# Kernel tuning notes

Measured on AMD Instinct MI355X. Metric: run time of the kernel, lower is better.

The kernel has to match this reference:

```python
import jax, jax.numpy as jnp
import numpy as np

EPS = 1e-7
LN_EPS = 1e-5

N_NODES = 50000
N_EDGES = 1600000
D = 128
L = 3


def layer_norm(h, scale, bias):
    mu = jnp.mean(h, axis=-1, keepdims=True)
    var = jnp.var(h, axis=-1, keepdims=True)
    return (h - mu) * jax.lax.rsqrt(var + LN_EPS) * scale + bias


def gen_conv(h, src, dst, edge_attr, W1, b1, W2, b2, beta, n_nodes):
    # message: ReLU(x_j + edge_attr) + eps   -> [E, D]
    msg = jax.nn.relu(h[src] + edge_attr) + EPS
    # softmax aggregation over incoming edges of each dst node, per feature
    s = beta * msg
    m = jax.ops.segment_max(s, dst, num_segments=n_nodes)  # [N, D]
    e = jnp.exp(s - m[dst])
    den = jax.ops.segment_sum(e, dst, num_segments=n_nodes)  # [N, D]
    alpha = e / den[dst]
    aggr = jax.ops.segment_sum(alpha * msg, dst, num_segments=n_nodes)  # [N, D]
    # MLP(x + aggr): D -> 2D -> D
    out = h + aggr
    out = jax.nn.relu(out @ W1 + b1)
    return out @ W2 + b2


def setup_inputs() -> dict:
    key = jax.random.key(0)
    ks = jax.random.split(key, 8)
    x = jax.random.normal(ks[0], (N_NODES, D), dtype=jnp.float32)
    edge_index = jax.random.randint(ks[1], (2, N_EDGES), 0, N_NODES, dtype=jnp.int64)
    edge_attr = jax.random.normal(ks[2], (N_EDGES, D), dtype=jnp.float32)
    return {
        "x": x,
        "edge_index": edge_index,
        "edge_attr": edge_attr,
        "ln_scale": jnp.ones((L, D), jnp.float32),
        "ln_bias": jnp.zeros((L, D), jnp.float32),
        "W1": jax.random.normal(ks[3], (L, D, 2 * D), jnp.float32) * 0.05,
        "b1": jnp.zeros((L, 2 * D), jnp.float32),
        "W2": jax.random.normal(ks[4], (L, 2 * D, D), jnp.float32) * 0.05,
        "b2": jnp.zeros((L, D), jnp.float32),
        "beta": jnp.ones((L,), jnp.float32),
        "lnf_scale": jnp.ones((D,), jnp.float32),
        "lnf_bias": jnp.zeros((D,), jnp.float32),
        "Wout": jax.random.normal(ks[5], (D, 1), jnp.float32) * 0.05,
        "bout": jnp.zeros((1,), jnp.float32),
    }


def reference(x, edge_index, edge_attr, ln_scale, ln_bias, W1, b1, W2, b2, beta,
              lnf_scale, lnf_bias, Wout, bout):
    src, dst = edge_index[0], edge_index[1]
    n = x.shape[0]
    # res+ DeeperGCN: first conv raw, then LN -> ReLU -> conv + residual
    h = gen_conv(x, src, dst, edge_attr, W1[0], b1[0], W2[0], b2[0], beta[0], n)
    for i in range(1, L):
        hn = jax.nn.relu(layer_norm(h, ln_scale[i], ln_bias[i]))
        h = gen_conv(hn, src, dst, edge_attr, W1[i], b1[i], W2[i], b2[i], beta[i], n) + h
    h = jax.nn.relu(layer_norm(h, lnf_scale, lnf_bias))
    return h @ Wout + bout
```

## Files before the change

### kernel.cpp

```cpp
#include <hip/hip_runtime.h>
#include <hip/hip_bf16.h>
#include <cstddef>

#define N_NODES 50000
#define N_EDGES 1600000
#define D 128
#define TWO_D 256
#define L 3
#define EPS 1e-7f
#define LN_EPS 1e-5f

typedef __attribute__((ext_vector_type(8))) short short8;
typedef __attribute__((ext_vector_type(4))) float f32x4;

__device__ __forceinline__ unsigned short f2bf(float f) {
    unsigned u = __float_as_uint(f);
    unsigned r = (u + 0x7fffu + ((u >> 16) & 1u)) >> 16;
    return (unsigned short)r;
}
__device__ __forceinline__ float bflo(unsigned u) { return __uint_as_float(u << 16); }
__device__ __forceinline__ float bfhi(unsigned u) { return __uint_as_float(u & 0xffff0000u); }
__device__ __forceinline__ unsigned bfpack(float lo, float hi) {
    return (unsigned)f2bf(lo) | ((unsigned)f2bf(hi) << 16);
}


__global__ __launch_bounds__(256) void hist_kernel(const int* __restrict__ ei, int* __restrict__ deg) {
    int idx = blockIdx.x * blockDim.x + threadIdx.x;
    int stride = gridDim.x * blockDim.x;
    for (int e = idx; e < N_EDGES; e += stride)
        atomicAdd(&deg[ei[N_EDGES + e]], 1);
}

__global__ __launch_bounds__(256) void scanA_kernel(const int* __restrict__ deg, int* __restrict__ part,
                                                    int* __restrict__ bsum) {
    __shared__ int wsum[4];
    int b = blockIdx.x, t = threadIdx.x;
    int lane = t & 63, wid = t >> 6;
    int base = b * 1024 + t * 4;
    int v0 = 0, v1 = 0, v2 = 0, v3 = 0;
    if (base + 0 < N_NODES) v0 = deg[base + 0];
    if (base + 1 < N_NODES) v1 = deg[base + 1];
    if (base + 2 < N_NODES) v2 = deg[base + 2];
    if (base + 3 < N_NODES) v3 = deg[base + 3];
    int s0 = v0, s1 = s0 + v1, s2 = s1 + v2, s3 = s2 + v3;
    int inc = s3;
    for (int off = 1; off < 64; off <<= 1) {
        int u = __shfl_up(inc, off);
        if (lane >= off) inc += u;
    }
    if (lane == 63) wsum[wid] = inc;
    __syncthreads();
    int woff = 0;
    for (int w = 0; w < wid; ++w) woff += wsum[w];
    int excl = woff + inc - s3;
    if (base + 0 < N_NODES) part[base + 0] = excl + s0;
    if (base + 1 < N_NODES) part[base + 1] = excl + s1;
    if (base + 2 < N_NODES) part[base + 2] = excl + s2;
    if (base + 3 < N_NODES) part[base + 3] = excl + s3;
    if (t == 255) bsum[b] = woff + inc;
}

__global__ __launch_bounds__(64) void scanB_kernel(int* __restrict__ bsum, int nb) {
    int lane = threadIdx.x;
    int v = (lane < nb) ? bsum[lane] : 0;
    int inc = v;
    for (int off = 1; off < 64; off <<= 1) {
        int u = __shfl_up(inc, off);
        if (lane >= off) inc += u;
    }
    if (lane < nb) bsum[lane] = inc - v;
}

__global__ __launch_bounds__(256) void scanC_kernel(const int* __restrict__ part, const int* __restrict__ bsum,
                                                    int* __restrict__ rowptr, int* __restrict__ cursor) {
    int i = blockIdx.x * blockDim.x + threadIdx.x;
    if (i >= N_NODES) return;
    rowptr[i + 1] = part[i] + bsum[i >> 10];
    cursor[i] = 0;
    if (i == 0) rowptr[0] = 0;
}

__global__ __launch_bounds__(256) void scatter_kernel(const int* __restrict__ ei, const int* __restrict__ rowptr,
                                                      int* __restrict__ cursor, int2* __restrict__ es2) {
    int idx = blockIdx.x * blockDim.x + threadIdx.x;
    int stride = gridDim.x * blockDim.x;
    for (int e = idx; e < N_EDGES; e += stride) {
        int dn = ei[N_EDGES + e];
        int pos = atomicAdd(&cursor[dn], 1);
        es2[rowptr[dn] + pos] = make_int2(ei[e], e);
    }
}

__global__ __launch_bounds__(256) void x2bf_kernel(const float* __restrict__ x, ushort2* __restrict__ xb) {
    int i = blockIdx.x * blockDim.x + threadIdx.x;
    if (i >= N_NODES * (D / 2)) return;
    float2 v = *(const float2*)(x + (size_t)i * 2);
    ushort2 o;
    o.x = f2bf(v.x);
    o.y = f2bf(v.y);
    xb[i] = o;
}

__global__ __launch_bounds__(256) void pack_w_kernel(const float* __restrict__ W1, const float* __restrict__ W2,
                                                     ushort* __restrict__ w1p, ushort* __restrict__ w2p) {
    int tid = blockIdx.x * 256 + threadIdx.x;
    if (tid >= 3 * 65536) return;
    int layer = tid >> 16, t2 = tid & 65535;
    if (t2 < 32768) {
        int j = t2 & 7, l = (t2 >> 3) & 63, kk = (t2 >> 9) & 3, ct = t2 >> 11;
        int k = kk * 32 + (l >> 4) * 8 + j, n = ct * 16 + (l & 15);
        w1p[(size_t)layer * 32768 + t2] = f2bf(W1[(size_t)layer * 32768 + k * 256 + n]);
    } else {
        int t3 = t2 - 32768;
        int j = t3 & 7, l = (t3 >> 3) & 63, kk = (t3 >> 9) & 7, ct = t3 >> 12;
        int k = kk * 32 + (l >> 4) * 8 + j, n = ct * 16 + (l & 15);
        w2p[(size_t)layer * 32768 + t3] = f2bf(W2[(size_t)layer * 32768 + k * 128 + n]);
    }
}


template <int PREP>
__global__ __launch_bounds__(256) void aggregate_kernel(const uint4* __restrict__ nodeb,
                                                        const float* __restrict__ ea,
                                                        ushort* __restrict__ eab,
                                                        const int* __restrict__ rowptr,
                                                        const int2* __restrict__ es2,
                                                        const float* __restrict__ beta, int layer,
                                                        ushort* __restrict__ preb) {
    int wid = threadIdx.x >> 6, lane = threadIdx.x & 63;
    int d = blockIdx.x * 4 + wid;
    if (d >= N_NODES) return;
    int e8 = lane >> 3;
    int f8 = lane & 7;
    float bet = beta[layer];
    int j0 = rowptr[d], j1 = rowptr[d + 1];
    int deg = j1 - j0;

    float se[16], sm[16];
#pragma unroll
    for (int i = 0; i < 16; ++i) { se[i] = 0.f; sm[i] = 0.f; }

    if (deg > 0) {
        int2 mp = (j0 + lane < j1) ? es2[j0 + lane] : make_int2(0, 0);
        bool small = (deg <= 64);
#pragma unroll 2
        for (int j = j0; j < j1; j += 8) {
            int e = j + e8;
            bool valid = e < j1;
            int ec = valid ? e : j1 - 1;
            int s, eid;
            if (small) {
                s   = __shfl(mp.x, ec - j0);
                eid = __shfl(mp.y, ec - j0);
            } else {
                int2 p = es2[ec];
                s = p.x; eid = p.y;
            }
            uint4 h0 = nodeb[(size_t)s * 16 + f8 * 2 + 0];
            uint4 h1 = nodeb[(size_t)s * 16 + f8 * 2 + 1];
            const unsigned* hu = (const unsigned*)&h0;
            const unsigned* hv = (const unsigned*)&h1;
            float vm = valid ? 1.f : 0.f;
            float af[16];
            if (PREP) {
                const float* ep = ea + (size_t)eid * D + f8 * 16;
                float4 fa0 = *(const float4*)(ep + 0);
                float4 fa1 = *(const float4*)(ep + 4);
                float4 fa2 = *(const float4*)(ep + 8);
                float4 fa3 = *(const float4*)(ep + 12);
                af[0] = fa0.x; af[1] = fa0.y; af[2] = fa0.z; af[3] = fa0.w;
                af[4] = fa1.x; af[5] = fa1.y; af[6] = fa1.z; af[7] = fa1.w;
                af[8] = fa2.x; af[9] = fa2.y; af[10] = fa2.z; af[11] = fa2.w;
                af[12] = fa3.x; af[13] = fa3.y; af[14] = fa3.z; af[15] = fa3.w;
                if (valid) {
                    uint4 o0, o1;
                    o0.x = bfpack(af[0], af[1]);  o0.y = bfpack(af[2], af[3]);
                    o0.z = bfpack(af[4], af[5]);  o0.w = bfpack(af[6], af[7]);
                    o1.x = bfpack(af[8], af[9]);  o1.y = bfpack(af[10], af[11]);
                    o1.z = bfpack(af[12], af[13]); o1.w = bfpack(af[14], af[15]);
                    uint4* dst = (uint4*)(eab + (size_t)ec * D + f8 * 16);
                    dst[0] = o0;
                    dst[1] = o1;
                }
            } else {
                uint4 a0 = *(const uint4*)(eab + (size_t)ec * D + f8 * 16);
                uint4 a1 = *(const uint4*)(eab + (size_t)ec * D + f8 * 16 + 8);
                const unsigned* au = (const unsigned*)&a0;
                const unsigned* av = (const unsigned*)&a1;
#pragma unroll
                for (int q = 0; q < 4; ++q) {
                    af[q * 2 + 0] = bflo(au[q]); af[q * 2 + 1] = bfhi(au[q]);
                    af[8 + q * 2 + 0] = bflo(av[q]); af[8 + q * 2 + 1] = bfhi(av[q]);
                }
            }
#pragma unroll
            for (int q = 0; q < 4; ++q) {
                float m0 = fmaxf(bflo(hu[q]) + af[q * 2 + 0], 0.f) + EPS;
                float m1 = fmaxf(bfhi(hu[q]) + af[q * 2 + 1], 0.f) + EPS;
                float ee0 = __expf(bet * m0) * vm;
                float ee1 = __expf(bet * m1) * vm;
                se[q * 2 + 0] += ee0; sm[q * 2 + 0] = fmaf(ee0, m0, sm[q * 2 + 0]);
                se[q * 2 + 1] += ee1; sm[q * 2 + 1] = fmaf(ee1, m1, sm[q * 2 + 1]);
            }
#pragma unroll
            for (int q = 0; q < 4; ++q) {
                float m0 = fmaxf(bflo(hv[q]) + af[8 + q * 2 + 0], 0.f) + EPS;
                float m1 = fmaxf(bfhi(hv[q]) + af[8 + q * 2 + 1], 0.f) + EPS;
                float ee0 = __expf(bet * m0) * vm;
                float ee1 = __expf(bet * m1) * vm;
                se[8 + q * 2 + 0] += ee0; sm[8 + q * 2 + 0] = fmaf(ee0, m0, sm[8 + q * 2 + 0]);
                se[8 + q * 2 + 1] += ee1; sm[8 + q * 2 + 1] = fmaf(ee1, m1, sm[8 + q * 2 + 1]);
            }
        }
    }

#pragma unroll
    for (int off = 8; off < 64; off <<= 1) {
#pragma unroll
        for (int i = 0; i < 16; ++i) {
            se[i] += __shfl_xor(se[i], off);
            sm[i] += __shfl_xor(sm[i], off);
        }
    }

    if (e8 == 0) {
        uint4 r0 = nodeb[(size_t)d * 16 + f8 * 2 + 0];
        uint4 r1 = nodeb[(size_t)d * 16 + f8 * 2 + 1];
        const unsigned* ru = (const unsigned*)&r0;
        const unsigned* rv = (const unsigned*)&r1;
        float v[16];
#pragma unroll
        for (int q = 0; q < 4; ++q) {
            v[q * 2 + 0] = bflo(ru[q]) + (se[q * 2 + 0] > 0.f ? sm[q * 2 + 0] / se[q * 2 + 0] : 0.f);
            v[q * 2 + 1] = bfhi(ru[q]) + (se[q * 2 + 1] > 0.f ? sm[q * 2 + 1] / se[q * 2 + 1] : 0.f);
            v[8 + q * 2 + 0] = bflo(rv[q]) + (se[8 + q * 2 + 0] > 0.f ? sm[8 + q * 2 + 0] / se[8 + q * 2 + 0] : 0.f);
            v[8 + q * 2 + 1] = bfhi(rv[q]) + (se[8 + q * 2 + 1] > 0.f ? sm[8 + q * 2 + 1] / se[8 + q * 2 + 1] : 0.f);
        }
        uint4 o0, o1;
        o0.x = bfpack(v[0], v[1]);   o0.y = bfpack(v[2], v[3]);
        o0.z = bfpack(v[4], v[5]);   o0.w = bfpack(v[6], v[7]);
        o1.x = bfpack(v[8], v[9]);   o1.y = bfpack(v[10], v[11]);
        o1.z = bfpack(v[12], v[13]); o1.w = bfpack(v[14], v[15]);
        uint4* dst = (uint4*)(preb + (size_t)d * D + f8 * 16);
        dst[0] = o0;
        dst[1] = o1;
    }
}


__global__ __launch_bounds__(256) void mlp_kernel(const ushort* __restrict__ preb,
                                                  const ushort* __restrict__ w1p, const float* __restrict__ b1,
                                                  const ushort* __restrict__ w2p, const float* __restrict__ b2,
                                                  const float* __restrict__ res,
                                                  float* __restrict__ h_out,
                                                  const float* __restrict__ ln_s, const float* __restrict__ ln_b,
                                                  ushort* __restrict__ hnb_out,
                                                  const float* __restrict__ Wout, const float* __restrict__ bout,
                                                  float* __restrict__ out, int mode) {
    __shared__ ushort hid[32][264];
    __shared__ float hid2[32][132];
    int t = threadIdx.x;
    int lane = t & 63, w = t >> 6;
    int rt = w & 1, ch = w >> 1;
    int node0 = blockIdx.x * 32;
    int l15 = lane & 15, l4 = lane >> 4;

    f32x4 acc[8];
#pragma unroll
    for (int ct = 0; ct < 8; ++ct) {
        float bb = b1[ch * 128 + ct * 16 + l15];
        f32x4 v = {bb, bb, bb, bb};
        acc[ct] = v;
    }
    const ushort* aprow = preb + (size_t)(node0 + rt * 16 + l15) * D + l4 * 8;
    const short8* w1f = (const short8*)w1p;
#pragma unroll
    for (int kk = 0; kk < 4; ++kk) {
        short8 a = *(const short8*)(aprow + kk * 32);
#pragma unroll
        for (int ct = 0; ct < 8; ++ct) {
            int ctg = ch * 8 + ct;
            short8 b = w1f[(ctg * 4 + kk) * 64 + lane];
            acc[ct] = __builtin_amdgcn_mfma_f32_16x16x32_bf16(a, b, acc[ct], 0, 0, 0);
        }
    }
#pragma unroll
    for (int ct = 0; ct < 8; ++ct) {
        int feat = ch * 128 + ct * 16 + l15;
        int row = rt * 16 + l4 * 4;
#pragma unroll
        for (int r = 0; r < 4; ++r)
            hid[row + r][feat] = f2bf(fmaxf(acc[ct][r], 0.f));
    }
    __syncthreads();

    f32x4 acc2[4];
#pragma unroll
    for (int ct = 0; ct < 4; ++ct) {
        f32x4 z = {0.f, 0.f, 0.f, 0.f};
        acc2[ct] = z;
    }
    const ushort* ahrow = &hid[rt * 16 + l15][l4 * 8];
    const short8* w2f = (const short8*)w2p;
#pragma unroll
    for (int kk = 0; kk < 8; ++kk) {
        short8 a = *(const short8*)(ahrow + kk * 32);
#pragma unroll
        for (int ct = 0; ct < 4; ++ct) {
            int ctg = ch * 4 + ct;
            short8 b = w2f[(ctg * 8 + kk) * 64 + lane];
            acc2[ct] = __builtin_amdgcn_mfma_f32_16x16x32_bf16(a, b, acc2[ct], 0, 0, 0);
        }
    }
#pragma unroll
    for (int ct = 0; ct < 4; ++ct) {
        int feat = ch * 64 + ct * 16 + l15;
        int row = rt * 16 + l4 * 4;
#pragma unroll
        for (int r = 0; r < 4; ++r)
            hid2[row + r][feat] = acc2[ct][r];
    }
    __syncthreads();

    int f4 = (t & 31) * 4;
    int ng = t >> 5;
    float4 b2v = *(const float4*)(b2 + f4);
#pragma unroll 1
    for (int n = 0; n < 4; ++n) {
        int nl = ng * 4 + n;
        int node = node0 + nl;
        bool valid = node < N_NODES;
        float4 v = *(float4*)&hid2[nl][f4];
        v.x += b2v.x; v.y += b2v.y; v.z += b2v.z; v.w += b2v.w;
        if (res != nullptr && valid) {
            float4 rv = *(const float4*)(res + (size_t)node * D + f4);
            v.x += rv.x; v.y += rv.y; v.z += rv.z; v.w += rv.w;
        }
        if (mode < 2 && valid) *(float4*)(h_out + (size_t)node * D + f4) = v;

        float s = v.x + v.y + v.z + v.w;
        for (int off = 16; off; off >>= 1) s += __shfl_xor(s, off);
        float mu = s * (1.0f / D);
        float dx = v.x - mu, dy = v.y - mu, dz = v.z - mu, dw = v.w - mu;
        float vs = dx * dx + dy * dy + dz * dz + dw * dw;
        for (int off = 16; off; off >>= 1) vs += __shfl_xor(vs, off);
        float r = rsqrtf(vs * (1.0f / D) + LN_EPS);
        float4 sc = *(const float4*)(ln_s + f4);
        float4 bi = *(const float4*)(ln_b + f4);
        float y0 = fmaxf(dx * r * sc.x + bi.x, 0.f);
        float y1 = fmaxf(dy * r * sc.y + bi.y, 0.f);
        float y2 = fmaxf(dz * r * sc.z + bi.z, 0.f);
        float y3 = fmaxf(dw * r * sc.w + bi.w, 0.f);
        if (mode < 2) {
            if (valid) {
                ushort4 hb;
                hb.x = f2bf(y0); hb.y = f2bf(y1); hb.z = f2bf(y2); hb.w = f2bf(y3);
                *(ushort4*)(hnb_out + (size_t)node * D + f4) = hb;
            }
        } else {
            float4 wv = *(const float4*)(Wout + f4);
            float dot = y0 * wv.x + y1 * wv.y + y2 * wv.z + y3 * wv.w;
            for (int off = 16; off; off >>= 1) dot += __shfl_xor(dot, off);
            if ((t & 31) == 0 && valid) out[node] = dot + bout[0];
        }
    }
}


extern "C" void kernel_launch(void* const* d_in, const int* in_sizes, int n_in,
                              void* d_out, int out_size, void* d_ws, size_t ws_size,
                              hipStream_t stream) {
    const float* x        = (const float*)d_in[0];
    const int*   ei       = (const int*)d_in[1];
    const float* ea       = (const float*)d_in[2];
    const float* ln_scale = (const float*)d_in[3];
    const float* ln_bias  = (const float*)d_in[4];
    const float* W1       = (const float*)d_in[5];
    const float* b1       = (const float*)d_in[6];
    const float* W2       = (const float*)d_in[7];
    const float* b2       = (const float*)d_in[8];
    const float* beta     = (const float*)d_in[9];
    const float* lnf_s    = (const float*)d_in[10];
    const float* lnf_b    = (const float*)d_in[11];
    const float* Wout     = (const float*)d_in[12];
    const float* bout     = (const float*)d_in[13];
    float* out = (float*)d_out;

    char* w = (char*)d_ws;
    float*  h    = (float*)w;  w += (size_t)N_NODES * D * 4;
    ushort* preb = (ushort*)w; w += (size_t)N_NODES * D * 2;
    ushort* hnb  = (ushort*)w; w += (size_t)N_NODES * D * 2;
    ushort* xb   = (ushort*)w; w += (size_t)N_NODES * D * 2;
    ushort* eab  = (ushort*)w; w += (size_t)N_EDGES * D * 2;
    int2* es2   = (int2*)w;  w += (size_t)N_EDGES * 8;
    ushort* w1p = (ushort*)w; w += (size_t)3 * 32768 * 2;
    ushort* w2p = (ushort*)w; w += (size_t)3 * 32768 * 2;
    int* deg    = (int*)w;   w += (size_t)N_NODES * 4;
    int* part   = (int*)w;   w += (size_t)50176 * 4;
    int* rowptr = (int*)w;   w += (size_t)(N_NODES + 1) * 4;
    int* cursor = (int*)w;   w += (size_t)N_NODES * 4;
    int* bsum   = (int*)w;   w += (size_t)64 * 4;

    const int NB = (N_NODES + 1023) / 1024;

    hipMemsetAsync(deg, 0, (size_t)N_NODES * 4, stream);
    hist_kernel<<<2048, 256, 0, stream>>>(ei, deg);
    scanA_kernel<<<NB, 256, 0, stream>>>(deg, part, bsum);
    scanB_kernel<<<1, 64, 0, stream>>>(bsum, NB);
    scanC_kernel<<<(N_NODES + 255) / 256, 256, 0, stream>>>(part, bsum, rowptr, cursor);
    scatter_kernel<<<2048, 256, 0, stream>>>(ei, rowptr, cursor, es2);
    x2bf_kernel<<<(N_NODES * (D / 2) + 255) / 256, 256, 0, stream>>>(x, (ushort2*)xb);
    pack_w_kernel<<<768, 256, 0, stream>>>(W1, W2, w1p, w2p);

    const int grid_rows = (N_NODES + 3) / 4;
    const int grid_gemm = (N_NODES + 31) / 32;

    for (int layer = 0; layer < L; ++layer) {
        const uint4* nodeb = (const uint4*)((layer == 0) ? xb : hnb);
        if (layer == 0)
            aggregate_kernel<1><<<grid_rows, 256, 0, stream>>>(nodeb, ea, eab, rowptr, es2, beta, layer, preb);
        else
            aggregate_kernel<0><<<grid_rows, 256, 0, stream>>>(nodeb, ea, eab, rowptr, es2, beta, layer, preb);

        if (layer < L - 1) {
            mlp_kernel<<<grid_gemm, 256, 0, stream>>>(preb,
                                                      w1p + (size_t)layer * 32768, b1 + (size_t)layer * TWO_D,
                                                      w2p + (size_t)layer * 32768, b2 + (size_t)layer * D,
                                                      layer == 0 ? nullptr : h, h,
                                                      ln_scale + (size_t)(layer + 1) * D,
                                                      ln_bias + (size_t)(layer + 1) * D,
                                                      hnb, nullptr, nullptr, nullptr, layer == 0 ? 0 : 1);
        } else {
            mlp_kernel<<<grid_gemm, 256, 0, stream>>>(preb,
                                                      w1p + (size_t)layer * 32768, b1 + (size_t)layer * TWO_D,
                                                      w2p + (size_t)layer * 32768, b2 + (size_t)layer * D,
                                                      h, nullptr,
                                                      lnf_s, lnf_b, nullptr,
                                                      Wout, bout, out, 2);
        }
    }
}
```

Measured before the change: 783.0 us.

## Fuse per-layer aggregation and MLP into one kernel with LDS staging

Merges the softmax-aggregation kernel and the MLP/LayerNorm kernel into a single per-layer kernel. Each 256-thread block aggregates 16 nodes into shared memory and runs both MFMA GEMMs on them from LDS, so the bf16 pre-MLP buffer no longer makes a global-memory round trip and one launch per layer is saved. Node features are ping-ponged between two buffers so a layer never overwrites the input that other blocks are still gathering. In exchange the GEMM tile drops from 32 to 16 rows, so weights are reloaded more often per node, and the aggregation loop now processes four nodes per wave serially.

```diff
diff --git a/kernel.cpp b/kernel.cpp
--- a/kernel.cpp
+++ b/kernel.cpp
@@ -12,6 +12,7 @@
 
 typedef __attribute__((ext_vector_type(8))) short short8;
 typedef __attribute__((ext_vector_type(4))) float f32x4;
+typedef __attribute__((ext_vector_type(4))) unsigned u32x4;
 
 __device__ __forceinline__ unsigned short f2bf(float f) {
     unsigned u = __float_as_uint(f);
@@ -121,202 +122,204 @@
 
 
 template <int PREP>
-__global__ __launch_bounds__(256) void aggregate_kernel(const uint4* __restrict__ nodeb,
-                                                        const float* __restrict__ ea,
-                                                        ushort* __restrict__ eab,
-                                                        const int* __restrict__ rowptr,
-                                                        const int2* __restrict__ es2,
-                                                        const float* __restrict__ beta, int layer,
-                                                        ushort* __restrict__ preb) {
-    int wid = threadIdx.x >> 6, lane = threadIdx.x & 63;
-    int d = blockIdx.x * 4 + wid;
-    if (d >= N_NODES) return;
+__global__ __launch_bounds__(256) void fused_layer_kernel(const uint4* __restrict__ nodeb,
+                                                          const float* __restrict__ ea,
+                                                          ushort* __restrict__ eab,
+                                                          const int* __restrict__ rowptr,
+                                                          const int2* __restrict__ es2,
+                                                          const float* __restrict__ beta, int layer,
+                                                          const ushort* __restrict__ w1p, const float* __restrict__ b1,
+                                                          const ushort* __restrict__ w2p, const float* __restrict__ b2,
+                                                          const float* __restrict__ res,
+                                                          float* __restrict__ h_out,
+                                                          const float* __restrict__ ln_s, const float* __restrict__ ln_b,
+                                                          ushort* __restrict__ hnb_out,
+                                                          const float* __restrict__ Wout, const float* __restrict__ bout,
+                                                          float* __restrict__ out, int mode) {
+    __shared__ ushort xs[16][136];
+    __shared__ ushort hid[16][264];
+    __shared__ float hid2[16][132];
+
+    int t = threadIdx.x;
+    int lane = t & 63, w = t >> 6;
+    int node0 = blockIdx.x * 16;
     int e8 = lane >> 3;
     int f8 = lane & 7;
+    int l15 = lane & 15, l4 = lane >> 4;
     float bet = beta[layer];
-    int j0 = rowptr[d], j1 = rowptr[d + 1];
-    int deg = j1 - j0;
-
-    float se[16], sm[16];
-#pragma unroll
-    for (int i = 0; i < 16; ++i) { se[i] = 0.f; sm[i] = 0.f; }
-
-    if (deg > 0) {
-        int2 mp = (j0 + lane < j1) ? es2[j0 + lane] : make_int2(0, 0);
-        bool small = (deg <= 64);
+
+    for (int i = 0; i < 4; ++i) {
+        int d = node0 + w * 4 + i;
+        int j0 = rowptr[d], j1 = rowptr[d + 1];
+        int deg = j1 - j0;
+
+        float se[16], sm[16];
+#pragma unroll
+        for (int q = 0; q < 16; ++q) { se[q] = 0.f; sm[q] = 0.f; }
+
+        if (deg > 0) {
+            int2 mp = (j0 + lane < j1) ? es2[j0 + lane] : make_int2(0, 0);
+            bool small = (deg <= 64);
 #pragma unroll 2
-        for (int j = j0; j < j1; j += 8) {
-            int e = j + e8;
-            bool valid = e < j1;
-            int ec = valid ? e : j1 - 1;
-            int s, eid;
-            if (small) {
-                s   = __shfl(mp.x, ec - j0);
-                eid = __shfl(mp.y, ec - j0);
-            } else {
-                int2 p = es2[ec];
-                s = p.x; eid = p.y;
-            }
-            uint4 h0 = nodeb[(size_t)s * 16 + f8 * 2 + 0];
-            uint4 h1 = nodeb[(size_t)s * 16 + f8 * 2 + 1];
-            const unsigned* hu = (const unsigned*)&h0;
-            const unsigned* hv = (const unsigned*)&h1;
-            float vm = valid ? 1.f : 0.f;
-            float af[16];
-            if (PREP) {
-                const float* ep = ea + (size_t)eid * D + f8 * 16;
-                float4 fa0 = *(const float4*)(ep + 0);
-                float4 fa1 = *(const float4*)(ep + 4);
-                float4 fa2 = *(const float4*)(ep + 8);
-                float4 fa3 = *(const float4*)(ep + 12);
-                af[0] = fa0.x; af[1] = fa0.y; af[2] = fa0.z; af[3] = fa0.w;
-                af[4] = fa1.x; af[5] = fa1.y; af[6] = fa1.z; af[7] = fa1.w;
-                af[8] = fa2.x; af[9] = fa2.y; af[10] = fa2.z; af[11] = fa2.w;
-                af[12] = fa3.x; af[13] = fa3.y; af[14] = fa3.z; af[15] = fa3.w;
-                if (valid) {
-                    uint4 o0, o1;
-                    o0.x = bfpack(af[0], af[1]);  o0.y = bfpack(af[2], af[3]);
-                    o0.z = bfpack(af[4], af[5]);  o0.w = bfpack(af[6], af[7]);
-                    o1.x = bfpack(af[8], af[9]);  o1.y = bfpack(af[10], af[11]);
-                    o1.z = bfpack(af[12], af[13]); o1.w = bfpack(af[14], af[15]);
-                    uint4* dst = (uint4*)(eab + (size_t)ec * D + f8 * 16);
-                    dst[0] = o0;
-                    dst[1] = o1;
+            for (int j = j0; j < j1; j += 8) {
+                int e = j + e8;
+                bool valid = e < j1;
+                int ec = valid ? e : j1 - 1;
+                int s, eid;
+                if (small) {
+                    s   = __shfl(mp.x, ec - j0);
+                    eid = __shfl(mp.y, ec - j0);
+                } else {
+                    int2 p = es2[ec];
+                    s = p.x; eid = p.y;
                 }
-            } else {
-                uint4 a0 = *(const uint4*)(eab + (size_t)ec * D + f8 * 16);
-                uint4 a1 = *(const uint4*)(eab + (size_t)ec * D + f8 * 16 + 8);
-                const unsigned* au = (const unsigned*)&a0;
-                const unsigned* av = (const unsigned*)&a1;
+                uint4 h0 = nodeb[(size_t)s * 16 + f8 * 2 + 0];
+                uint4 h1 = nodeb[(size_t)s * 16 + f8 * 2 + 1];
+                const unsigned* hu = (const unsigned*)&h0;
+                const unsigned* hv = (const unsigned*)&h1;
+                float vm = valid ? 1.f : 0.f;
+                float af[16];
+                if (PREP) {
+                    const float* ep = ea + (size_t)eid * D + f8 * 16;
+                    f32x4 fa0 = *(const f32x4*)(ep + 0);
+                    f32x4 fa1 = *(const f32x4*)(ep + 4);
+                    f32x4 fa2 = *(const f32x4*)(ep + 8);
+                    f32x4 fa3 = *(const f32x4*)(ep + 12);
+#pragma unroll
+                    for (int q = 0; q < 4; ++q) {
+                        af[q] = fa0[q];
+                        af[4 + q] = fa1[q];
+                        af[8 + q] = fa2[q];
+                        af[12 + q] = fa3[q];
+                    }
+                    if (valid) {
+                        u32x4 o0, o1;
+                        o0[0] = bfpack(af[0], af[1]);  o0[1] = bfpack(af[2], af[3]);
+                        o0[2] = bfpack(af[4], af[5]);  o0[3] = bfpack(af[6], af[7]);
+                        o1[0] = bfpack(af[8], af[9]);  o1[1] = bfpack(af[10], af[11]);
+                        o1[2] = bfpack(af[12], af[13]); o1[3] = bfpack(af[14], af[15]);
+                        u32x4* dst = (u32x4*)(eab + (size_t)ec * D + f8 * 16);
+                        dst[0] = o0;
+                        dst[1] = o1;
+                    }
+                } else {
+                    const u32x4* ap = (const u32x4*)(eab + (size_t)ec * D + f8 * 16);
+                    u32x4 a0 = ap[0];
+                    u32x4 a1 = ap[1];
+#pragma unroll
+                    for (int q = 0; q < 4; ++q) {
+                        af[q * 2 + 0] = bflo(a0[q]); af[q * 2 + 1] = bfhi(a0[q]);
+                        af[8 + q * 2 + 0] = bflo(a1[q]); af[8 + q * 2 + 1] = bfhi(a1[q]);
+                    }
+                }
 #pragma unroll
                 for (int q = 0; q < 4; ++q) {
-                    af[q * 2 + 0] = bflo(au[q]); af[q * 2 + 1] = bfhi(au[q]);
-                    af[8 + q * 2 + 0] = bflo(av[q]); af[8 + q * 2 + 1] = bfhi(av[q]);
+                    float m0 = fmaxf(bflo(hu[q]) + af[q * 2 + 0], 0.f) + EPS;
+                    float m1 = fmaxf(bfhi(hu[q]) + af[q * 2 + 1], 0.f) + EPS;
+                    float ee0 = __expf(bet * m0) * vm;
+                    float ee1 = __expf(bet * m1) * vm;
+                    se[q * 2 + 0] += ee0; sm[q * 2 + 0] = fmaf(ee0, m0, sm[q * 2 + 0]);
+                    se[q * 2 + 1] += ee1; sm[q * 2 + 1] = fmaf(ee1, m1, sm[q * 2 + 1]);
+                }
+#pragma unroll
+                for (int q = 0; q < 4; ++q) {
+                    float m0 = fmaxf(bflo(hv[q]) + af[8 + q * 2 + 0], 0.f) + EPS;
+                    float m1 = fmaxf(bfhi(hv[q]) + af[8 + q * 2 + 1], 0.f) + EPS;
+                    float ee0 = __expf(bet * m0) * vm;
+                    float ee1 = __expf(bet * m1) * vm;
+                    se[8 + q * 2 + 0] += ee0; sm[8 + q * 2 + 0] = fmaf(ee0, m0, sm[8 + q * 2 + 0]);
+                    se[8 + q * 2 + 1] += ee1; sm[8 + q * 2 + 1] = fmaf(ee1, m1, sm[8 + q * 2 + 1]);
                 }
             }
+        }
+
+#pragma unroll
+        for (int off = 8; off < 64; off <<= 1) {
+#pragma unroll
+            for (int q = 0; q < 16; ++q) {
+                se[q] += __shfl_xor(se[q], off);
+                sm[q] += __shfl_xor(sm[q], off);
+            }
+        }
+
+        if (e8 == 0) {
+            uint4 r0 = nodeb[(size_t)d * 16 + f8 * 2 + 0];
+            uint4 r1 = nodeb[(size_t)d * 16 + f8 * 2 + 1];
+            const unsigned* ru = (const unsigned*)&r0;
+            const unsigned* rv = (const unsigned*)&r1;
+            float v[16];
 #pragma unroll
             for (int q = 0; q < 4; ++q) {
-                float m0 = fmaxf(bflo(hu[q]) + af[q * 2 + 0], 0.f) + EPS;
-                float m1 = fmaxf(bfhi(hu[q]) + af[q * 2 + 1], 0.f) + EPS;
-                float ee0 = __expf(bet * m0) * vm;
-                float ee1 = __expf(bet * m1) * vm;
-                se[q * 2 + 0] += ee0; sm[q * 2 + 0] = fmaf(ee0, m0, sm[q * 2 + 0]);
-                se[q * 2 + 1] += ee1; sm[q * 2 + 1] = fmaf(ee1, m1, sm[q * 2 + 1]);
+                v[q * 2 + 0] = bflo(ru[q]) + (se[q * 2 + 0] > 0.f ? sm[q * 2 + 0] / se[q * 2 + 0] : 0.f);
+                v[q * 2 + 1] = bfhi(ru[q]) + (se[q * 2 + 1] > 0.f ? sm[q * 2 + 1] / se[q * 2 + 1] : 0.f);
+                v[8 + q * 2 + 0] = bflo(rv[q]) + (se[8 + q * 2 + 0] > 0.f ? sm[8 + q * 2 + 0] / se[8 + q * 2 + 0] : 0.f);
+                v[8 + q * 2 + 1] = bfhi(rv[q]) + (se[8 + q * 2 + 1] > 0.f ? sm[8 + q * 2 + 1] / se[8 + q * 2 + 1] : 0.f);
             }
-#pragma unroll
-            for (int q = 0; q < 4; ++q) {
-                float m0 = fmaxf(bflo(hv[q]) + af[8 + q * 2 + 0], 0.f) + EPS;
-                float m1 = fmaxf(bfhi(hv[q]) + af[8 + q * 2 + 1], 0.f) + EPS;
-                float ee0 = __expf(bet * m0) * vm;
-                float ee1 = __expf(bet * m1) * vm;
-                se[8 + q * 2 + 0] += ee0; sm[8 + q * 2 + 0] = fmaf(ee0, m0, sm[8 + q * 2 + 0]);
-                se[8 + q * 2 + 1] += ee1; sm[8 + q * 2 + 1] = fmaf(ee1, m1, sm[8 + q * 2 + 1]);
-            }
-        }
-    }
-
-#pragma unroll
-    for (int off = 8; off < 64; off <<= 1) {
-#pragma unroll
-        for (int i = 0; i < 16; ++i) {
-            se[i] += __shfl_xor(se[i], off);
-            sm[i] += __shfl_xor(sm[i], off);
-        }
-    }
-
-    if (e8 == 0) {
-        uint4 r0 = nodeb[(size_t)d * 16 + f8 * 2 + 0];
-        uint4 r1 = nodeb[(size_t)d * 16 + f8 * 2 + 1];
-        const unsigned* ru = (const unsigned*)&r0;
-        const unsigned* rv = (const unsigned*)&r1;
-        float v[16];
-#pragma unroll
-        for (int q = 0; q < 4; ++q) {
-            v[q * 2 + 0] = bflo(ru[q]) + (se[q * 2 + 0] > 0.f ? sm[q * 2 + 0] / se[q * 2 + 0] : 0.f);
-            v[q * 2 + 1] = bfhi(ru[q]) + (se[q * 2 + 1] > 0.f ? sm[q * 2 + 1] / se[q * 2 + 1] : 0.f);
-            v[8 + q * 2 + 0] = bflo(rv[q]) + (se[8 + q * 2 + 0] > 0.f ? sm[8 + q * 2 + 0] / se[8 + q * 2 + 0] : 0.f);
-            v[8 + q * 2 + 1] = bfhi(rv[q]) + (se[8 + q * 2 + 1] > 0.f ? sm[8 + q * 2 + 1] / se[8 + q * 2 + 1] : 0.f);
-        }
-        uint4 o0, o1;
-        o0.x = bfpack(v[0], v[1]);   o0.y = bfpack(v[2], v[3]);
-        o0.z = bfpack(v[4], v[5]);   o0.w = bfpack(v[6], v[7]);
-        o1.x = bfpack(v[8], v[9]);   o1.y = bfpack(v[10], v[11]);
-        o1.z = bfpack(v[12], v[13]); o1.w = bfpack(v[14], v[15]);
-        uint4* dst = (uint4*)(preb + (size_t)d * D + f8 * 16);
-        dst[0] = o0;
-        dst[1] = o1;
-    }
-}
-
-
-__global__ __launch_bounds__(256) void mlp_kernel(const ushort* __restrict__ preb,
-                                                  const ushort* __restrict__ w1p, const float* __restrict__ b1,
-                                                  const ushort* __restrict__ w2p, const float* __restrict__ b2,
-                                                  const float* __restrict__ res,
-                                                  float* __restrict__ h_out,
-                                                  const float* __restrict__ ln_s, const float* __restrict__ ln_b,
-                                                  ushort* __restrict__ hnb_out,
-                                                  const float* __restrict__ Wout, const float* __restrict__ bout,
-                                                  float* __restrict__ out, int mode) {
-    __shared__ ushort hid[32][264];
-    __shared__ float hid2[32][132];
-    int t = threadIdx.x;
-    int lane = t & 63, w = t >> 6;
-    int rt = w & 1, ch = w >> 1;
-    int node0 = blockIdx.x * 32;
-    int l15 = lane & 15, l4 = lane >> 4;
-
-    f32x4 acc[8];
-#pragma unroll
-    for (int ct = 0; ct < 8; ++ct) {
-        float bb = b1[ch * 128 + ct * 16 + l15];
+            int nl = w * 4 + i;
+            uint4 o0, o1;
+            o0.x = bfpack(v[0], v[1]);   o0.y = bfpack(v[2], v[3]);
+            o0.z = bfpack(v[4], v[5]);   o0.w = bfpack(v[6], v[7]);
+            o1.x = bfpack(v[8], v[9]);   o1.y = bfpack(v[10], v[11]);
+            o1.z = bfpack(v[12], v[13]); o1.w = bfpack(v[14], v[15]);
+            uint4* dst = (uint4*)&xs[nl][f8 * 16];
+            dst[0] = o0;
+            dst[1] = o1;
+        }
+    }
+    __syncthreads();
+
+    f32x4 acc[4];
+#pragma unroll
+    for (int ct = 0; ct < 4; ++ct) {
+        int ctg = w * 4 + ct;
+        float bb = b1[ctg * 16 + l15];
         f32x4 v = {bb, bb, bb, bb};
         acc[ct] = v;
     }
-    const ushort* aprow = preb + (size_t)(node0 + rt * 16 + l15) * D + l4 * 8;
+    const ushort* aprow = &xs[l15][l4 * 8];
     const short8* w1f = (const short8*)w1p;
 #pragma unroll
     for (int kk = 0; kk < 4; ++kk) {
         short8 a = *(const short8*)(aprow + kk * 32);
 #pragma unroll
-        for (int ct = 0; ct < 8; ++ct) {
-            int ctg = ch * 8 + ct;
+        for (int ct = 0; ct < 4; ++ct) {
+            int ctg = w * 4 + ct;
             short8 b = w1f[(ctg * 4 + kk) * 64 + lane];
             acc[ct] = __builtin_amdgcn_mfma_f32_16x16x32_bf16(a, b, acc[ct], 0, 0, 0);
         }
     }
 #pragma unroll
-    for (int ct = 0; ct < 8; ++ct) {
-        int feat = ch * 128 + ct * 16 + l15;
-        int row = rt * 16 + l4 * 4;
+    for (int ct = 0; ct < 4; ++ct) {
+        int feat = w * 64 + ct * 16 + l15;
+        int row = l4 * 4;
 #pragma unroll
         for (int r = 0; r < 4; ++r)
             hid[row + r][feat] = f2bf(fmaxf(acc[ct][r], 0.f));
     }
     __syncthreads();
 
-    f32x4 acc2[4];
-#pragma unroll
-    for (int ct = 0; ct < 4; ++ct) {
+    f32x4 acc2[2];
+#pragma unroll
+    for (int ct = 0; ct < 2; ++ct) {
         f32x4 z = {0.f, 0.f, 0.f, 0.f};
         acc2[ct] = z;
     }
-    const ushort* ahrow = &hid[rt * 16 + l15][l4 * 8];
+    const ushort* ahrow = &hid[l15][l4 * 8];
     const short8* w2f = (const short8*)w2p;
 #pragma unroll
     for (int kk = 0; kk < 8; ++kk) {
         short8 a = *(const short8*)(ahrow + kk * 32);
 #pragma unroll
-        for (int ct = 0; ct < 4; ++ct) {
-            int ctg = ch * 4 + ct;
+        for (int ct = 0; ct < 2; ++ct) {
+            int ctg = w * 2 + ct;
             short8 b = w2f[(ctg * 8 + kk) * 64 + lane];
             acc2[ct] = __builtin_amdgcn_mfma_f32_16x16x32_bf16(a, b, acc2[ct], 0, 0, 0);
         }
     }
 #pragma unroll
-    for (int ct = 0; ct < 4; ++ct) {
-        int feat = ch * 64 + ct * 16 + l15;
-        int row = rt * 16 + l4 * 4;
+    for (int ct = 0; ct < 2; ++ct) {
+        int feat = w * 32 + ct * 16 + l15;
+        int row = l4 * 4;
 #pragma unroll
         for (int r = 0; r < 4; ++r)
             hid2[row + r][feat] = acc2[ct][r];
@@ -327,17 +330,16 @@
     int ng = t >> 5;
     float4 b2v = *(const float4*)(b2 + f4);
 #pragma unroll 1
-    for (int n = 0; n < 4; ++n) {
-        int nl = ng * 4 + n;
+    for (int n = 0; n < 2; ++n) {
+        int nl = ng * 2 + n;
         int node = node0 + nl;
-        bool valid = node < N_NODES;
         float4 v = *(float4*)&hid2[nl][f4];
         v.x += b2v.x; v.y += b2v.y; v.z += b2v.z; v.w += b2v.w;
-        if (res != nullptr && valid) {
+        if (res != nullptr) {
             float4 rv = *(const float4*)(res + (size_t)node * D + f4);
             v.x += rv.x; v.y += rv.y; v.z += rv.z; v.w += rv.w;
         }
-        if (mode < 2 && valid) *(float4*)(h_out + (size_t)node * D + f4) = v;
+        if (mode < 2) *(float4*)(h_out + (size_t)node * D + f4) = v;
 
         float s = v.x + v.y + v.z + v.w;
         for (int off = 16; off; off >>= 1) s += __shfl_xor(s, off);
@@ -353,16 +355,14 @@
         float y2 = fmaxf(dz * r * sc.z + bi.z, 0.f);
         float y3 = fmaxf(dw * r * sc.w + bi.w, 0.f);
         if (mode < 2) {
-            if (valid) {
-                ushort4 hb;
-                hb.x = f2bf(y0); hb.y = f2bf(y1); hb.z = f2bf(y2); hb.w = f2bf(y3);
-                *(ushort4*)(hnb_out + (size_t)node * D + f4) = hb;
-            }
+            ushort4 hb;
+            hb.x = f2bf(y0); hb.y = f2bf(y1); hb.z = f2bf(y2); hb.w = f2bf(y3);
+            *(ushort4*)(hnb_out + (size_t)node * D + f4) = hb;
         } else {
             float4 wv = *(const float4*)(Wout + f4);
             float dot = y0 * wv.x + y1 * wv.y + y2 * wv.z + y3 * wv.w;
             for (int off = 16; off; off >>= 1) dot += __shfl_xor(dot, off);
-            if ((t & 31) == 0 && valid) out[node] = dot + bout[0];
+            if ((t & 31) == 0) out[node] = dot + bout[0];
         }
     }
 }
@@ -389,8 +389,8 @@
 
     char* w = (char*)d_ws;
     float*  h    = (float*)w;  w += (size_t)N_NODES * D * 4;
-    ushort* preb = (ushort*)w; w += (size_t)N_NODES * D * 2;
-    ushort* hnb  = (ushort*)w; w += (size_t)N_NODES * D * 2;
+    ushort* hnbA = (ushort*)w; w += (size_t)N_NODES * D * 2;
+    ushort* hnbB = (ushort*)w; w += (size_t)N_NODES * D * 2;
     ushort* xb   = (ushort*)w; w += (size_t)N_NODES * D * 2;
     ushort* eab  = (ushort*)w; w += (size_t)N_EDGES * D * 2;
     int2* es2   = (int2*)w;  w += (size_t)N_EDGES * 8;
@@ -413,31 +413,21 @@
     x2bf_kernel<<<(N_NODES * (D / 2) + 255) / 256, 256, 0, stream>>>(x, (ushort2*)xb);
     pack_w_kernel<<<768, 256, 0, stream>>>(W1, W2, w1p, w2p);
 
-    const int grid_rows = (N_NODES + 3) / 4;
-    const int grid_gemm = (N_NODES + 31) / 32;
-
-    for (int layer = 0; layer < L; ++layer) {
-        const uint4* nodeb = (const uint4*)((layer == 0) ? xb : hnb);
-        if (layer == 0)
-            aggregate_kernel<1><<<grid_rows, 256, 0, stream>>>(nodeb, ea, eab, rowptr, es2, beta, layer, preb);
-        else
-            aggregate_kernel<0><<<grid_rows, 256, 0, stream>>>(nodeb, ea, eab, rowptr, es2, beta, layer, preb);
-
-        if (layer < L - 1) {
-            mlp_kernel<<<grid_gemm, 256, 0, stream>>>(preb,
-                                                      w1p + (size_t)layer * 32768, b1 + (size_t)layer * TWO_D,
-                                                      w2p + (size_t)layer * 32768, b2 + (size_t)layer * D,
-                                                      layer == 0 ? nullptr : h, h,
-                                                      ln_scale + (size_t)(layer + 1) * D,
-                                                      ln_bias + (size_t)(layer + 1) * D,
-                                                      hnb, nullptr, nullptr, nullptr, layer == 0 ? 0 : 1);
-        } else {
-            mlp_kernel<<<grid_gemm, 256, 0, stream>>>(preb,
-                                                      w1p + (size_t)layer * 32768, b1 + (size_t)layer * TWO_D,
-                                                      w2p + (size_t)layer * 32768, b2 + (size_t)layer * D,
-                                                      h, nullptr,
-                                                      lnf_s, lnf_b, nullptr,
-                                                      Wout, bout, out, 2);
-        }
-    }
-}
+    const int grid_fused = N_NODES / 16;
+
+    fused_layer_kernel<1><<<grid_fused, 256, 0, stream>>>(
+        (const uint4*)xb, ea, eab, rowptr, es2, beta, 0,
+        w1p, b1, w2p, b2,
+        nullptr, h, ln_scale + (size_t)1 * D, ln_bias + (size_t)1 * D,
+        hnbA, nullptr, nullptr, nullptr, 0);
+    fused_layer_kernel<0><<<grid_fused, 256, 0, stream>>>(
+        (const uint4*)hnbA, ea, eab, rowptr, es2, beta, 1,
+        w1p + 32768, b1 + TWO_D, w2p + 32768, b2 + D,
+        h, h, ln_scale + (size_t)2 * D, ln_bias + (size_t)2 * D,
+        hnbB, nullptr, nullptr, nullptr, 1);
+    fused_layer_kernel<0><<<grid_fused, 256, 0, stream>>>(
+        (const uint4*)hnbB, ea, eab, rowptr, es2, beta, 2,
+        w1p + 65536, b1 + 2 * TWO_D, w2p + 65536, b2 + 2 * D,
+        h, nullptr, lnf_s, lnf_b,
+        nullptr, Wout, bout, out, 2);
+}
```

Result: slower. 814.3 us (+4.0%).
